# Performance work log

Hardware: AMD Instinct MI355X
Metric: run time of the kernel (lower is better)

## Reference

```python
import jax, jax.numpy as jnp
import numpy as np

N_NODES = 100000
N_EDGES = 1600000
MIN_NORM = 1e-15
BALL_EPS = 1e-5  # stay strictly inside the unit ball


def _norm(x):
    return jnp.linalg.norm(x, axis=-1, keepdims=True)


def artanh(x):
    return jnp.arctanh(jnp.clip(x, -1.0 + BALL_EPS, 1.0 - BALL_EPS))


def proj(x):
    n = jnp.maximum(_norm(x), MIN_NORM)
    maxn = 1.0 - BALL_EPS
    return jnp.where(n > maxn, x / n * maxn, x)


def expmap0(u):
    n = jnp.maximum(_norm(u), MIN_NORM)
    return jnp.tanh(n) * u / n


def logmap0(x):
    n = jnp.maximum(_norm(x), MIN_NORM)
    return artanh(n) * x / n


def mobius_add(x, y):
    x2 = jnp.sum(x * x, -1, keepdims=True)
    y2 = jnp.sum(y * y, -1, keepdims=True)
    xy = jnp.sum(x * y, -1, keepdims=True)
    num = (1.0 + 2.0 * xy + y2) * x + (1.0 - x2) * y
    den = 1.0 + 2.0 * xy + x2 * y2
    return num / jnp.maximum(den, MIN_NORM)


def mobius_matvec(W, x):
    mx = x @ W.T
    xn = jnp.maximum(_norm(x), MIN_NORM)
    mxn = jnp.maximum(_norm(mx), MIN_NORM)
    return jnp.tanh(mxn / xn * artanh(xn)) * mx / mxn


def hyp_layer(x, W, b, edge_index, use_act, use_agg):
    h = proj(mobius_matvec(W, x))
    h = proj(mobius_add(h, expmap0(b)[None, :]))
    if use_agg:
        src, dst = edge_index[0], edge_index[1]
        t = logmap0(h)                       # tangent space at origin
        msg = t[src]                         # [E, d] gather
        agg = jax.ops.segment_sum(msg, dst, num_segments=N_NODES)
        deg = jax.ops.segment_sum(jnp.ones((edge_index.shape[1],), t.dtype),
                                  dst, num_segments=N_NODES)
        agg = agg / jnp.maximum(deg, 1.0)[:, None]   # mean aggregation
        h = proj(expmap0(agg))
    if use_act:
        h = proj(expmap0(jax.nn.relu(logmap0(h))))
    return h


def lorentz_to_poincare(x):
    return x[:, 1:] / (x[:, :1] + 1.0)


def setup_inputs() -> dict:
    key = jax.random.key(0)
    ks = jax.random.split(key, 16)
    d_in, h1, d_out = 64, 64, 32
    # valid hyperboloid points: x0 = sqrt(1 + |xs|^2)
    xs = 0.1 * jax.random.normal(ks[0], (N_NODES, d_in - 1), jnp.float32)
    x0 = jnp.sqrt(1.0 + jnp.sum(xs * xs, -1, keepdims=True))
    x = jnp.concatenate([x0, xs], axis=-1)
    edge_index = jax.random.randint(ks[1], (2, N_EDGES), 0, N_NODES, jnp.int64)

    def lin(k, o, i):
        return jax.random.normal(k, (o, i), jnp.float32) * (1.0 / np.sqrt(i))

    return {
        "x": x,
        "W1": lin(ks[2], h1, d_in - 1), "b1": jnp.zeros((h1,), jnp.float32),
        "W2": lin(ks[3], h1, h1),       "b2": jnp.zeros((h1,), jnp.float32),
        "W3": lin(ks[4], h1, h1),       "b3": jnp.zeros((h1,), jnp.float32),
        "W4": lin(ks[5], h1, h1),       "b4": jnp.zeros((h1,), jnp.float32),
        "W5": lin(ks[6], h1, h1),       "b5": jnp.zeros((h1,), jnp.float32),
        "W6": lin(ks[7], d_out, h1),    "b6": jnp.zeros((d_out,), jnp.float32),
        "edge_index": edge_index,
    }


def reference(x, W1, b1, W2, b2, W3, b3, W4, b4, W5, b5, W6, b6, edge_index):
    h = proj(lorentz_to_poincare(x))
    h = hyp_layer(h, W1, b1, edge_index, use_act=True,  use_agg=False)  # hconv1
    h = hyp_layer(h, W2, b2, edge_index, use_act=True,  use_agg=False)  # hconv_2
    h = hyp_layer(h, W3, b3, edge_index, use_act=True,  use_agg=False)  # hconv_3
    h = hyp_layer(h, W4, b4, edge_index, use_act=True,  use_agg=True)   # hconv2
    h = hyp_layer(h, W5, b5, edge_index, use_act=True,  use_agg=True)   # hconv3
    h = hyp_layer(h, W6, b6, edge_index, use_act=False, use_agg=False)  # hconv4
    return h
```

## Files before the change

kernel.cpp:

```cpp
#include <hip/hip_runtime.h>
#include <hip/hip_fp16.h>

#define NN 100000
#define NE 1600000
#define TILES 6250
#define MIN_NORM 1e-15f
#define BALL_EPS 1e-5f
#define MAXN (1.0f - BALL_EPS)

#define BSH 9
#define NB 196
#define CH 8192
#define MAXB 16384

typedef __attribute__((ext_vector_type(8))) short bf16x8;
typedef __attribute__((ext_vector_type(4))) float f32x4;


__device__ __forceinline__ float rcpf(float x) { return __builtin_amdgcn_rcpf(x); }

__device__ __forceinline__ float ftanh(float x) {
    float e = __expf(-2.0f * x);
    return (1.0f - e) * rcpf(1.0f + e);
}

__device__ __forceinline__ float fatanh_c(float x) {
    x = fminf(fmaxf(x, -MAXN), MAXN);
    return 0.5f * __logf((1.0f + x) * rcpf(1.0f - x));
}


__device__ __forceinline__ float wred(float x) {
    int t;
    t = __builtin_amdgcn_update_dpp(0, __float_as_int(x), 0x111, 0xf, 0xf, false);
    x += __int_as_float(t);
    t = __builtin_amdgcn_update_dpp(0, __float_as_int(x), 0x112, 0xf, 0xf, false);
    x += __int_as_float(t);
    t = __builtin_amdgcn_update_dpp(0, __float_as_int(x), 0x114, 0xf, 0xf, false);
    x += __int_as_float(t);
    t = __builtin_amdgcn_update_dpp(0, __float_as_int(x), 0x118, 0xf, 0xf, false);
    x += __int_as_float(t);
    t = __builtin_amdgcn_update_dpp(0, __float_as_int(x), 0x142, 0xa, 0xf, false);
    x += __int_as_float(t);
    t = __builtin_amdgcn_update_dpp(0, __float_as_int(x), 0x143, 0xc, 0xf, false);
    x += __int_as_float(t);
    return __int_as_float(__builtin_amdgcn_readlane(__float_as_int(x), 63));
}

__device__ __forceinline__ float red16(float x) {
    int t;
    t = __builtin_amdgcn_update_dpp(0, __float_as_int(x), 0xB1, 0xf, 0xf, false);
    x += __int_as_float(t);
    t = __builtin_amdgcn_update_dpp(0, __float_as_int(x), 0x4E, 0xf, 0xf, false);
    x += __int_as_float(t);
    t = __builtin_amdgcn_ds_swizzle(__float_as_int(x), 0x101F);
    x += __int_as_float(t);
    t = __builtin_amdgcn_ds_swizzle(__float_as_int(x), 0x201F);
    x += __int_as_float(t);
    return x;
}


__global__ __launch_bounds__(256) void prep_w(const float* __restrict__ W1,
                                              const float* __restrict__ W2,
                                              const float* __restrict__ W3,
                                              const float* __restrict__ W4,
                                              const float* __restrict__ W5,
                                              const float* __restrict__ W6,
                                              short* __restrict__ wsplit) {
    int m = blockIdx.y;
    const float* Ws[6] = {W1, W2, W3, W4, W5, W6};
    const int dins[6] = {63, 64, 64, 64, 64, 64};
    const int douts[6] = {64, 64, 64, 64, 64, 32};
    const float* W = Ws[m];
    int din = dins[m], dout = douts[m];
    int idx = blockIdx.x * 256 + threadIdx.x;
    int j = idx >> 6, k = idx & 63;
    float x = (j < dout && k < din) ? W[j * din + k] : 0.0f;
    unsigned u = __float_as_uint(x);
    float r = x - __uint_as_float(u & 0xFFFF0000u);
    wsplit[m * 8192 + idx] = (short)(u >> 16);
    wsplit[m * 8192 + 4096 + idx] = (short)(__float_as_uint(r) >> 16);
}


__global__ __launch_bounds__(256) void l2p_kernel(const float* __restrict__ x,
                                                  float* __restrict__ out) {
    int lane = threadIdx.x & 63;
    int gw = blockIdx.x * (blockDim.x >> 6) + (threadIdx.x >> 6);
    int nw = gridDim.x * (blockDim.x >> 6);
    for (int node = gw; node < NN; node += nw) {
        float x0 = x[node * 64];
        float p = 0.0f;
        if (lane < 63) p = x[node * 64 + 1 + lane] * rcpf(x0 + 1.0f);
        float n = fmaxf(sqrtf(wred(p * p)), MIN_NORM);
        if (n > MAXN) p = p * (MAXN * rcpf(n));
        out[node * 64 + lane] = p;
    }
}

template <int MODE, int NT>
__global__ __launch_bounds__(256, 3) void layer_mfma(const float* __restrict__ in,
                                                     const short* __restrict__ wsp,
                                                     const float* __restrict__ b,
                                                     void* __restrict__ outv) {
    const int dout = NT * 16;
    float* outf = (float*)outv;
    __half* outh = (__half*)outv;
    int tid = threadIdx.x;
    int lane = tid & 63;
    int q = lane >> 4;
    int m15 = lane & 15;
    int wv = (blockIdx.x * 256 + tid) >> 6;
    int nwave = (gridDim.x * 256) >> 6;

    bf16x8 wb1[NT][2], wb2[NT][2];
#pragma unroll
    for (int t = 0; t < NT; ++t)
#pragma unroll
        for (int s = 0; s < 2; ++s) {
            int off = (16 * t + m15) * 64 + 32 * s + 8 * q;
            wb1[t][s] = *(const bf16x8*)(wsp + off);
            wb2[t][s] = *(const bf16x8*)(wsp + 4096 + off);
        }

    float bv[NT], bp = 0.0f;
#pragma unroll
    for (int t = 0; t < NT; ++t) {
        bv[t] = b[16 * t + m15];
        bp = fmaf(bv[t], bv[t], bp);
    }
    float bsum = red16(bp);
    bool bnz = (bsum > 0.0f);
    float ybt[NT] = {}; float y2 = 0.0f;
    if (bnz) {
        float bn = fmaxf(sqrtf(bsum), MIN_NORM);
        float fy = ftanh(bn) * rcpf(bn);
#pragma unroll
        for (int t = 0; t < NT; ++t) ybt[t] = fy * bv[t];
        y2 = fy * fy * bsum;
    }

    for (int tt = wv; tt < TILES; tt += nwave) {
        int base = tt * 16;
        const float* vrow = in + (size_t)(base + m15) * 64;

        bf16x8 a1[2], a2[2];
        float svp = 0.0f;
#pragma unroll
        for (int s = 0; s < 2; ++s) {
            float4 u0 = *(const float4*)(vrow + 32 * s + 8 * q);
            float4 u1 = *(const float4*)(vrow + 32 * s + 8 * q + 4);
            float f[8] = {u0.x, u0.y, u0.z, u0.w, u1.x, u1.y, u1.z, u1.w};
#pragma unroll
            for (int j = 0; j < 8; ++j) {
                svp = fmaf(f[j], f[j], svp);
                unsigned u = __float_as_uint(f[j]);
                a1[s][j] = (short)(u >> 16);
                float r = f[j] - __uint_as_float(u & 0xFFFF0000u);
                a2[s][j] = (short)(__float_as_uint(r) >> 16);
            }
        }
        float sv = svp;
        sv += __shfl_xor(sv, 16);
        sv += __shfl_xor(sv, 32);

        f32x4 acc[NT];
#pragma unroll
        for (int t = 0; t < NT; ++t) acc[t] = (f32x4){0.f, 0.f, 0.f, 0.f};
#pragma unroll
        for (int t = 0; t < NT; ++t)
#pragma unroll
            for (int s = 0; s < 2; ++s) {
                acc[t] = __builtin_amdgcn_mfma_f32_16x16x32_bf16(a1[s], wb1[t][s], acc[t], 0, 0, 0);
                acc[t] = __builtin_amdgcn_mfma_f32_16x16x32_bf16(a1[s], wb2[t][s], acc[t], 0, 0, 0);
                acc[t] = __builtin_amdgcn_mfma_f32_16x16x32_bf16(a2[s], wb1[t][s], acc[t], 0, 0, 0);
            }

        float sm[4], svr[4];
#pragma unroll
        for (int r = 0; r < 4; ++r) {
            float p = 0.0f;
#pragma unroll
            for (int t = 0; t < NT; ++t) p = fmaf(acc[t][r], acc[t][r], p);
            sm[r] = red16(p);
            svr[r] = __shfl(sv, 4 * q + r);
        }

        float o[NT][4];
#pragma unroll
        for (int r = 0; r < 4; ++r) {
            float xn = fmaxf(sqrtf(svr[r]), MIN_NORM);
            float mxn = fmaxf(sqrtf(sm[r]), MIN_NORM);
            float s1 = fminf(ftanh(mxn * rcpf(xn) * fatanh_c(xn)), MAXN);
            float fr = s1 * rcpf(mxn);
            float hv[NT];
#pragma unroll
            for (int t = 0; t < NT; ++t) hv[t] = acc[t][r] * fr;
            float hn = s1;

            if (bnz) {
                float hp = 0.0f;
#pragma unroll
                for (int t = 0; t < NT; ++t) hp = fmaf(hv[t], ybt[t], hp);
                float hy = red16(hp);
                float h2 = s1 * s1;
                float den = fmaxf(1.0f + 2.0f * hy + h2 * y2, MIN_NORM);
                float rd = rcpf(den);
                float cA = (1.0f + 2.0f * hy + y2) * rd;
                float cB = (1.0f - h2) * rd;
                float hq = 0.0f;
#pragma unroll
                for (int t = 0; t < NT; ++t) {
                    hv[t] = cA * hv[t] + cB * ybt[t];
                    hq = fmaf(hv[t], hv[t], hq);
                }
                hn = fmaxf(sqrtf(red16(hq)), MIN_NORM);
            }

            if (MODE == 2) {
                float f2 = fminf(hn, MAXN) * rcpf(hn);
#pragma unroll
                for (int t = 0; t < NT; ++t) o[t][r] = hv[t] * f2;
            } else {
                float nn = fminf(hn, MAXN);
                float tf = fatanh_c(nn) * rcpf(hn);
                if (MODE == 1) {
#pragma unroll
                    for (int t = 0; t < NT; ++t) o[t][r] = tf * hv[t];
                } else {
                    float tv[NT], tp = 0.0f;
#pragma unroll
                    for (int t = 0; t < NT; ++t) {
                        tv[t] = fmaxf(tf * hv[t], 0.0f);
                        tp = fmaf(tv[t], tv[t], tp);
                    }
                    float tn = fmaxf(sqrtf(red16(tp)), MIN_NORM);
                    float g = fminf(ftanh(tn), MAXN) * rcpf(tn);
#pragma unroll
                    for (int t = 0; t < NT; ++t) o[t][r] = tv[t] * g;
                }
            }
        }

        if (MODE == 1) {
#pragma unroll
            for (int t = 0; t < NT; ++t)
#pragma unroll
                for (int r = 0; r < 4; ++r)
                    outh[(size_t)(base + 4 * q + r) * 64 + 16 * t + m15] = __float2half(o[t][r]);
        } else {
#pragma unroll
            for (int t = 0; t < NT; ++t)
#pragma unroll
                for (int r = 0; r < 4; ++r)
                    outf[(size_t)(base + 4 * q + r) * dout + 16 * t + m15] = o[t][r];
        }
    }
}


__global__ __launch_bounds__(256) void p0_hist(const int* __restrict__ ei,
                                               int* __restrict__ ghist) {
    __shared__ int h[NB];
    for (int i = threadIdx.x; i < NB; i += 256) h[i] = 0;
    __syncthreads();
    int stride = gridDim.x * 256;
    for (int e = blockIdx.x * 256 + threadIdx.x; e < NE; e += stride)
        atomicAdd(&h[ei[NE + e] >> BSH], 1);
    __syncthreads();
    for (int i = threadIdx.x; i < NB; i += 256)
        if (h[i]) atomicAdd(&ghist[i], h[i]);
}

__global__ __launch_bounds__(256) void p_scan(const int* __restrict__ ghist,
                                              int* __restrict__ boff,
                                              int* __restrict__ bcur,
                                              int* __restrict__ rowptr) {
    __shared__ int lds[256];
    int t = threadIdx.x;
    int v = (t < NB) ? ghist[t] : 0;
    lds[t] = v;
    __syncthreads();
    for (int off = 1; off < 256; off <<= 1) {
        int u = (t >= off) ? lds[t - off] : 0;
        __syncthreads();
        lds[t] += u;
        __syncthreads();
    }
    if (t < NB) { boff[t] = lds[t] - v; bcur[t] = lds[t] - v; }
    if (t == NB - 1) boff[NB] = lds[t];
    if (t == 0) rowptr[NN] = NE;
}

__global__ __launch_bounds__(256) void p1_part(const int* __restrict__ ei,
                                               int* __restrict__ bcur,
                                               unsigned* __restrict__ packed) {
    __shared__ int hist[NB], excl[NB], cur[NB], gbase[NB];
    __shared__ int scan[256];
    __shared__ unsigned buf[CH];
    __shared__ unsigned char bseg[CH];
    int t = threadIdx.x;
    int e0 = blockIdx.x * CH;
    int n = min(CH, NE - e0);

    for (int i = t; i < NB; i += 256) hist[i] = 0;
    __syncthreads();
    for (int i = t; i < n; i += 256)
        atomicAdd(&hist[ei[NE + e0 + i] >> BSH], 1);
    __syncthreads();
    int v = (t < NB) ? hist[t] : 0;
    scan[t] = v;
    __syncthreads();
    for (int off = 1; off < 256; off <<= 1) {
        int u = (t >= off) ? scan[t - off] : 0;
        __syncthreads();
        scan[t] += u;
        __syncthreads();
    }
    if (t < NB) {
        excl[t] = scan[t] - v;
        cur[t] = scan[t] - v;
        gbase[t] = v ? atomicAdd(&bcur[t], v) : 0;
    }
    __syncthreads();
    for (int i = t; i < n; i += 256) {
        int src = ei[e0 + i], dst = ei[NE + e0 + i];
        int b = dst >> BSH;
        int p = atomicAdd(&cur[b], 1);
        buf[p] = ((unsigned)(dst & 511) << 17) | (unsigned)src;
        bseg[p] = (unsigned char)b;
    }
    __syncthreads();
    for (int i = t; i < n; i += 256) {
        int b = bseg[i];
        packed[gbase[b] + (i - excl[b])] = buf[i];
    }
}

__global__ __launch_bounds__(512) void p2_csr(const unsigned* __restrict__ packed,
                                              const int* __restrict__ boff,
                                              int* __restrict__ rowptr,
                                              int* __restrict__ csr) {
    __shared__ int lh[512], lex[512], lcur[512], scan[512];
    __shared__ int image[MAXB];
    int t = threadIdx.x;
    int b = blockIdx.x;
    int n0 = b << BSH;
    int nn = min(512, NN - n0);
    int ebeg = boff[b], eend = boff[b + 1];
    int cnt = eend - ebeg;

    lh[t] = 0;
    __syncthreads();
    for (int i = t; i < cnt; i += 512)
        atomicAdd(&lh[packed[ebeg + i] >> 17], 1);
    __syncthreads();
    int v = lh[t];
    scan[t] = v;
    __syncthreads();
    for (int off = 1; off < 512; off <<= 1) {
        int u = (t >= off) ? scan[t - off] : 0;
        __syncthreads();
        scan[t] += u;
        __syncthreads();
    }
    lex[t] = scan[t] - v;
    lcur[t] = scan[t] - v;
    if (t < nn) rowptr[n0 + t] = ebeg + lex[t];
    __syncthreads();
    for (int i = t; i < cnt; i += 512) {
        unsigned p = packed[ebeg + i];
        int pos = atomicAdd(&lcur[p >> 17], 1);
        image[pos] = (int)(p & 0x1FFFFu);
    }
    __syncthreads();
    for (int i = t; i < cnt; i += 512)
        csr[ebeg + i] = image[i];
}


__global__ __launch_bounds__(256) void gather_post_kernel(const __half* __restrict__ t16,
                                                          const int* __restrict__ rowptr,
                                                          const int* __restrict__ csr,
                                                          float* __restrict__ out) {
    int lane = threadIdx.x & 63;
    int g = lane >> 4;
    int l16 = lane & 15;
    int dq = l16 << 2;
    int gw = blockIdx.x * (blockDim.x >> 6) + (threadIdx.x >> 6);
    int nw = gridDim.x * (blockDim.x >> 6);
    for (int node = gw; node < NN; node += nw) {
        int beg = __builtin_amdgcn_readfirstlane(rowptr[node]);
        int end = __builtin_amdgcn_readfirstlane(rowptr[node + 1]);
        float ax = 0.f, ay = 0.f, az = 0.f, aw = 0.f;
        float bx = 0.f, by = 0.f, bz = 0.f, bw = 0.f;
        int i = beg;
        for (; i + 8 <= end; i += 8) {
            int sA = csr[i + g];
            int sB = csr[i + 4 + g];
            uint2 uA = *(const uint2*)(t16 + ((sA << 6) + dq));
            uint2 uB = *(const uint2*)(t16 + ((sB << 6) + dq));
            float2 fA0 = __half22float2(*(const half2*)&uA.x);
            float2 fA1 = __half22float2(*(const half2*)&uA.y);
            float2 fB0 = __half22float2(*(const half2*)&uB.x);
            float2 fB1 = __half22float2(*(const half2*)&uB.y);
            ax += fA0.x; ay += fA0.y; az += fA1.x; aw += fA1.y;
            bx += fB0.x; by += fB0.y; bz += fB1.x; bw += fB1.y;
        }
        for (; i < end; i += 4) {
            int idx = i + g;
            if (idx < end) {
                int s = csr[idx];
                uint2 u = *(const uint2*)(t16 + ((s << 6) + dq));
                float2 f0 = __half22float2(*(const half2*)&u.x);
                float2 f1 = __half22float2(*(const half2*)&u.y);
                ax += f0.x; ay += f0.y; az += f1.x; aw += f1.y;
            }
        }
        ax += bx; ay += by; az += bz; aw += bw;
        ax += __shfl_xor(ax, 16); ax += __shfl_xor(ax, 32);
        ay += __shfl_xor(ay, 16); ay += __shfl_xor(ay, 32);
        az += __shfl_xor(az, 16); az += __shfl_xor(az, 32);
        aw += __shfl_xor(aw, 16); aw += __shfl_xor(aw, 32);
        float rdeg = rcpf(fmaxf((float)(end - beg), 1.0f));
        ax *= rdeg; ay *= rdeg; az *= rdeg; aw *= rdeg;

        float p = fmaf(ax, ax, fmaf(ay, ay, fmaf(az, az, aw * aw)));
        p = red16(p);
        float n = fmaxf(sqrtf(p), MIN_NORM);
        float s = fminf(ftanh(n), MAXN);
        float c = fatanh_c(s) * rcpf(s) * (s * rcpf(n));
        float tx = fmaxf(c * ax, 0.f), ty = fmaxf(c * ay, 0.f);
        float tz = fmaxf(c * az, 0.f), tw = fmaxf(c * aw, 0.f);
        float tp = fmaf(tx, tx, fmaf(ty, ty, fmaf(tz, tz, tw * tw)));
        tp = red16(tp);
        float tn = fmaxf(sqrtf(tp), MIN_NORM);
        float g2 = fminf(ftanh(tn), MAXN) * rcpf(tn);
        if (g == 0) {
            float4 o = {tx * g2, ty * g2, tz * g2, tw * g2};
            *(float4*)(out + (size_t)node * 64 + dq) = o;
        }
    }
}


extern "C" void kernel_launch(void* const* d_in, const int* in_sizes, int n_in,
                              void* d_out, int out_size, void* d_ws, size_t ws_size,
                              hipStream_t stream) {
    const float* x  = (const float*)d_in[0];
    const float* W1 = (const float*)d_in[1];  const float* b1 = (const float*)d_in[2];
    const float* W2 = (const float*)d_in[3];  const float* b2 = (const float*)d_in[4];
    const float* W3 = (const float*)d_in[5];  const float* b3 = (const float*)d_in[6];
    const float* W4 = (const float*)d_in[7];  const float* b4 = (const float*)d_in[8];
    const float* W5 = (const float*)d_in[9];  const float* b5 = (const float*)d_in[10];
    const float* W6 = (const float*)d_in[11]; const float* b6 = (const float*)d_in[12];
    const int*   ei = (const int*)d_in[13];
    float* out = (float*)d_out;

    float*    A      = (float*)d_ws;
    float*    B      = A + (size_t)NN * 64;
    __half*   T16    = (__half*)(B + (size_t)NN * 64);
    int*      csr    = (int*)(T16 + (size_t)NN * 64);
    int*      rowptr = csr + NE;
    unsigned* packed = (unsigned*)(rowptr + NN + 1);
    int*      ghist  = (int*)(packed + NE);
    int*      boff   = ghist + NB;
    int*      bcur   = boff + NB + 1;
    short*    wsplit = (short*)(bcur + NB);

    dim3 blk(256);
    const int lg = 768;
    const int ng = 1024;
    const int gg = 2048;
    const int p1g = (NE + CH - 1) / CH;

    prep_w<<<dim3(16, 6), blk, 0, stream>>>(W1, W2, W3, W4, W5, W6, wsplit);
    hipMemsetAsync(ghist, 0, NB * sizeof(int), stream);
    p0_hist<<<512, blk, 0, stream>>>(ei, ghist);
    p_scan<<<1, blk, 0, stream>>>(ghist, boff, bcur, rowptr);
    p1_part<<<p1g, blk, 0, stream>>>(ei, bcur, packed);
    p2_csr<<<NB, 512, 0, stream>>>(packed, boff, rowptr, csr);

    l2p_kernel<<<ng, blk, 0, stream>>>(x, A);

    layer_mfma<0, 4><<<lg, blk, 0, stream>>>(A, wsplit + 0 * 8192, b1, B);
    layer_mfma<0, 4><<<lg, blk, 0, stream>>>(B, wsplit + 1 * 8192, b2, A);
    layer_mfma<0, 4><<<lg, blk, 0, stream>>>(A, wsplit + 2 * 8192, b3, B);

    layer_mfma<1, 4><<<lg, blk, 0, stream>>>(B, wsplit + 3 * 8192, b4, T16);
    gather_post_kernel<<<gg, blk, 0, stream>>>(T16, rowptr, csr, B);

    layer_mfma<1, 4><<<lg, blk, 0, stream>>>(B, wsplit + 4 * 8192, b5, T16);
    gather_post_kernel<<<gg, blk, 0, stream>>>(T16, rowptr, csr, B);

    layer_mfma<2, 2><<<lg, blk, 0, stream>>>(B, wsplit + 5 * 8192, b6, out);
}
```

Before: 364.4 us.

## Store activations as pre-split bf16 hi/lo with cached norms and artanh

Inter-layer activations are now written as pre-split bf16 hi/lo planes plus a per-node (norm, artanh(norm)) pair, so each layer loads MFMA operands directly instead of reloading fp32 and splitting them. The norm and artanh are computed once by the producer. The code also uses the algebraic identity artanh(tanh(z)) = z, clamped at ZMAX, to skip the tanh/artanh round trips when the bias is zero and in the gather epilogue. The split does not change activation bytes and adds a small norm side buffer. The shortcut depends on the clamp constant matching the reference clipping, and the packed buffer now aliases T16.

```diff
diff --git a/kernel.cpp b/kernel.cpp
--- a/kernel.cpp
+++ b/kernel.cpp
@@ -7,6 +7,7 @@
 #define MIN_NORM 1e-15f
 #define BALL_EPS 1e-5f
 #define MAXN (1.0f - BALL_EPS)
+#define ZMAX 6.1030338f
 
 #define BSH 9
 #define NB 196
@@ -14,6 +15,7 @@
 #define MAXB 16384
 
 typedef __attribute__((ext_vector_type(8))) short bf16x8;
+typedef __attribute__((ext_vector_type(4))) short short4v;
 typedef __attribute__((ext_vector_type(4))) float f32x4;
 
 
@@ -27,6 +29,13 @@
 __device__ __forceinline__ float fatanh_c(float x) {
     x = fminf(fmaxf(x, -MAXN), MAXN);
     return 0.5f * __logf((1.0f + x) * rcpf(1.0f - x));
+}
+
+__device__ __forceinline__ void bsplit(float v, short& hi, short& lo) {
+    unsigned u = __float_as_uint(v);
+    hi = (short)(u >> 16);
+    float r = v - __uint_as_float(u & 0xFFFF0000u);
+    lo = (short)(__float_as_uint(r) >> 16);
 }
 
 
@@ -77,15 +86,17 @@
     int idx = blockIdx.x * 256 + threadIdx.x;
     int j = idx >> 6, k = idx & 63;
     float x = (j < dout && k < din) ? W[j * din + k] : 0.0f;
-    unsigned u = __float_as_uint(x);
-    float r = x - __uint_as_float(u & 0xFFFF0000u);
-    wsplit[m * 8192 + idx] = (short)(u >> 16);
-    wsplit[m * 8192 + 4096 + idx] = (short)(__float_as_uint(r) >> 16);
+    short hi, lo;
+    bsplit(x, hi, lo);
+    wsplit[m * 8192 + idx] = hi;
+    wsplit[m * 8192 + 4096 + idx] = lo;
 }
 
 
 __global__ __launch_bounds__(256) void l2p_kernel(const float* __restrict__ x,
-                                                  float* __restrict__ out) {
+                                                  short* __restrict__ outHi,
+                                                  short* __restrict__ outLo,
+                                                  float2* __restrict__ outNrm) {
     int lane = threadIdx.x & 63;
     int gw = blockIdx.x * (blockDim.x >> 6) + (threadIdx.x >> 6);
     int nw = gridDim.x * (blockDim.x >> 6);
@@ -95,18 +106,29 @@
         if (lane < 63) p = x[node * 64 + 1 + lane] * rcpf(x0 + 1.0f);
         float n = fmaxf(sqrtf(wred(p * p)), MIN_NORM);
         if (n > MAXN) p = p * (MAXN * rcpf(n));
-        out[node * 64 + lane] = p;
+        short hi, lo;
+        bsplit(p, hi, lo);
+        outHi[node * 64 + lane] = hi;
+        outLo[node * 64 + lane] = lo;
+        if (lane == 0) {
+            float xn = fminf(n, MAXN);
+            outNrm[node] = make_float2(xn, fatanh_c(xn));
+        }
     }
 }
 
 template <int MODE, int NT>
-__global__ __launch_bounds__(256, 3) void layer_mfma(const float* __restrict__ in,
+__global__ __launch_bounds__(256, 3) void layer_mfma(const short* __restrict__ inHi,
+                                                     const short* __restrict__ inLo,
+                                                     const float2* __restrict__ inNrm,
                                                      const short* __restrict__ wsp,
                                                      const float* __restrict__ b,
-                                                     void* __restrict__ outv) {
+                                                     short* __restrict__ outHi,
+                                                     short* __restrict__ outLo,
+                                                     float2* __restrict__ outNrm,
+                                                     __half* __restrict__ outT,
+                                                     float* __restrict__ outF) {
     const int dout = NT * 16;
-    float* outf = (float*)outv;
-    __half* outh = (__half*)outv;
     int tid = threadIdx.x;
     int lane = tid & 63;
     int q = lane >> 4;
@@ -143,27 +165,15 @@
 
     for (int tt = wv; tt < TILES; tt += nwave) {
         int base = tt * 16;
-        const float* vrow = in + (size_t)(base + m15) * 64;
+        int rowoff = (base + m15) * 64;
 
         bf16x8 a1[2], a2[2];
-        float svp = 0.0f;
 #pragma unroll
         for (int s = 0; s < 2; ++s) {
-            float4 u0 = *(const float4*)(vrow + 32 * s + 8 * q);
-            float4 u1 = *(const float4*)(vrow + 32 * s + 8 * q + 4);
-            float f[8] = {u0.x, u0.y, u0.z, u0.w, u1.x, u1.y, u1.z, u1.w};
-#pragma unroll
-            for (int j = 0; j < 8; ++j) {
-                svp = fmaf(f[j], f[j], svp);
-                unsigned u = __float_as_uint(f[j]);
-                a1[s][j] = (short)(u >> 16);
-                float r = f[j] - __uint_as_float(u & 0xFFFF0000u);
-                a2[s][j] = (short)(__float_as_uint(r) >> 16);
-            }
-        }
-        float sv = svp;
-        sv += __shfl_xor(sv, 16);
-        sv += __shfl_xor(sv, 32);
+            a1[s] = *(const bf16x8*)(inHi + rowoff + 32 * s + 8 * q);
+            a2[s] = *(const bf16x8*)(inLo + rowoff + 32 * s + 8 * q);
+        }
+        float2 nrm = inNrm[base + m15];
 
         f32x4 acc[NT];
 #pragma unroll
@@ -177,34 +187,73 @@
                 acc[t] = __builtin_amdgcn_mfma_f32_16x16x32_bf16(a2[s], wb1[t][s], acc[t], 0, 0, 0);
             }
 
-        float sm[4], svr[4];
+        float sm[4];
 #pragma unroll
         for (int r = 0; r < 4; ++r) {
             float p = 0.0f;
 #pragma unroll
             for (int t = 0; t < NT; ++t) p = fmaf(acc[t][r], acc[t][r], p);
             sm[r] = red16(p);
-            svr[r] = __shfl(sv, 4 * q + r);
-        }
-
-        float o[NT][4];
+        }
+
 #pragma unroll
         for (int r = 0; r < 4; ++r) {
-            float xn = fmaxf(sqrtf(svr[r]), MIN_NORM);
+            int nd = base + 4 * q + r;
+            float xn = __shfl(nrm.x, 4 * q + r);
+            float axn = __shfl(nrm.y, 4 * q + r);
             float mxn = fmaxf(sqrtf(sm[r]), MIN_NORM);
-            float s1 = fminf(ftanh(mxn * rcpf(xn) * fatanh_c(xn)), MAXN);
-            float fr = s1 * rcpf(mxn);
-            float hv[NT];
-#pragma unroll
-            for (int t = 0; t < NT; ++t) hv[t] = acc[t][r] * fr;
-            float hn = s1;
-
-            if (bnz) {
+            float z = mxn * rcpf(xn) * axn;
+            float az = fminf(z, ZMAX);
+
+            if (!bnz) {
+                if (MODE == 2) {
+                    float e = __expf(-2.0f * z);
+                    float s1c = fminf((1.0f - e) * rcpf(1.0f + e), MAXN);
+                    float fr = s1c * rcpf(mxn);
+#pragma unroll
+                    for (int t = 0; t < NT; ++t)
+                        outF[(size_t)nd * dout + 16 * t + m15] = acc[t][r] * fr;
+                } else {
+                    float tfac = az * rcpf(mxn);
+                    if (MODE == 1) {
+#pragma unroll
+                        for (int t = 0; t < NT; ++t)
+                            outT[(size_t)nd * 64 + 16 * t + m15] = __float2half(tfac * acc[t][r]);
+                    } else {
+                        float tv[NT], tp = 0.0f;
+#pragma unroll
+                        for (int t = 0; t < NT; ++t) {
+                            tv[t] = fmaxf(tfac * acc[t][r], 0.0f);
+                            tp = fmaf(tv[t], tv[t], tp);
+                        }
+                        float tn = fmaxf(sqrtf(red16(tp)), MIN_NORM);
+                        float e2 = __expf(-2.0f * tn);
+                        float s2c = fminf((1.0f - e2) * rcpf(1.0f + e2), MAXN);
+                        float g = s2c * rcpf(tn);
+#pragma unroll
+                        for (int t = 0; t < NT; ++t) {
+                            short hi, lo;
+                            bsplit(tv[t] * g, hi, lo);
+                            int idx = nd * 64 + 16 * t + m15;
+                            outHi[idx] = hi;
+                            outLo[idx] = lo;
+                        }
+                        if (m15 == 0)
+                            outNrm[nd] = make_float2(fmaxf(s2c, MIN_NORM), fminf(tn, ZMAX));
+                    }
+                }
+            } else {
+                float e = __expf(-2.0f * z);
+                float s1c = fminf((1.0f - e) * rcpf(1.0f + e), MAXN);
+                float fr = s1c * rcpf(mxn);
+                float hv[NT];
+#pragma unroll
+                for (int t = 0; t < NT; ++t) hv[t] = acc[t][r] * fr;
                 float hp = 0.0f;
 #pragma unroll
                 for (int t = 0; t < NT; ++t) hp = fmaf(hv[t], ybt[t], hp);
                 float hy = red16(hp);
-                float h2 = s1 * s1;
+                float h2 = s1c * s1c;
                 float den = fmaxf(1.0f + 2.0f * hy + h2 * y2, MIN_NORM);
                 float rd = rcpf(den);
                 float cA = (1.0f + 2.0f * hy + y2) * rd;
@@ -215,46 +264,41 @@
                     hv[t] = cA * hv[t] + cB * ybt[t];
                     hq = fmaf(hv[t], hv[t], hq);
                 }
-                hn = fmaxf(sqrtf(red16(hq)), MIN_NORM);
-            }
-
-            if (MODE == 2) {
-                float f2 = fminf(hn, MAXN) * rcpf(hn);
-#pragma unroll
-                for (int t = 0; t < NT; ++t) o[t][r] = hv[t] * f2;
-            } else {
-                float nn = fminf(hn, MAXN);
-                float tf = fatanh_c(nn) * rcpf(hn);
-                if (MODE == 1) {
-#pragma unroll
-                    for (int t = 0; t < NT; ++t) o[t][r] = tf * hv[t];
+                float hn = fmaxf(sqrtf(red16(hq)), MIN_NORM);
+                if (MODE == 2) {
+                    float f2 = fminf(hn, MAXN) * rcpf(hn);
+#pragma unroll
+                    for (int t = 0; t < NT; ++t)
+                        outF[(size_t)nd * dout + 16 * t + m15] = hv[t] * f2;
                 } else {
-                    float tv[NT], tp = 0.0f;
-#pragma unroll
-                    for (int t = 0; t < NT; ++t) {
-                        tv[t] = fmaxf(tf * hv[t], 0.0f);
-                        tp = fmaf(tv[t], tv[t], tp);
+                    float tf = fatanh_c(fminf(hn, MAXN)) * rcpf(hn);
+                    if (MODE == 1) {
+#pragma unroll
+                        for (int t = 0; t < NT; ++t)
+                            outT[(size_t)nd * 64 + 16 * t + m15] = __float2half(tf * hv[t]);
+                    } else {
+                        float tv[NT], tp = 0.0f;
+#pragma unroll
+                        for (int t = 0; t < NT; ++t) {
+                            tv[t] = fmaxf(tf * hv[t], 0.0f);
+                            tp = fmaf(tv[t], tv[t], tp);
+                        }
+                        float tn = fmaxf(sqrtf(red16(tp)), MIN_NORM);
+                        float s2c = fminf(ftanh(tn), MAXN);
+                        float g = s2c * rcpf(tn);
+#pragma unroll
+                        for (int t = 0; t < NT; ++t) {
+                            short hi, lo;
+                            bsplit(tv[t] * g, hi, lo);
+                            int idx = nd * 64 + 16 * t + m15;
+                            outHi[idx] = hi;
+                            outLo[idx] = lo;
+                        }
+                        if (m15 == 0)
+                            outNrm[nd] = make_float2(fmaxf(s2c, MIN_NORM), fminf(tn, ZMAX));
                     }
-                    float tn = fmaxf(sqrtf(red16(tp)), MIN_NORM);
-                    float g = fminf(ftanh(tn), MAXN) * rcpf(tn);
-#pragma unroll
-                    for (int t = 0; t < NT; ++t) o[t][r] = tv[t] * g;
                 }
             }
-        }
-
-        if (MODE == 1) {
-#pragma unroll
-            for (int t = 0; t < NT; ++t)
-#pragma unroll
-                for (int r = 0; r < 4; ++r)
-                    outh[(size_t)(base + 4 * q + r) * 64 + 16 * t + m15] = __float2half(o[t][r]);
-        } else {
-#pragma unroll
-            for (int t = 0; t < NT; ++t)
-#pragma unroll
-                for (int r = 0; r < 4; ++r)
-                    outf[(size_t)(base + 4 * q + r) * dout + 16 * t + m15] = o[t][r];
         }
     }
 }
@@ -383,7 +427,9 @@
 __global__ __launch_bounds__(256) void gather_post_kernel(const __half* __restrict__ t16,
                                                           const int* __restrict__ rowptr,
                                                           const int* __restrict__ csr,
-                                                          float* __restrict__ out) {
+                                                          short* __restrict__ outHi,
+                                                          short* __restrict__ outLo,
+                                                          float2* __restrict__ outNrm) {
     int lane = threadIdx.x & 63;
     int g = lane >> 4;
     int l16 = lane & 15;
@@ -429,17 +475,24 @@
         float p = fmaf(ax, ax, fmaf(ay, ay, fmaf(az, az, aw * aw)));
         p = red16(p);
         float n = fmaxf(sqrtf(p), MIN_NORM);
-        float s = fminf(ftanh(n), MAXN);
-        float c = fatanh_c(s) * rcpf(s) * (s * rcpf(n));
+        float c = (n > ZMAX) ? (ZMAX * rcpf(n)) : 1.0f;
         float tx = fmaxf(c * ax, 0.f), ty = fmaxf(c * ay, 0.f);
         float tz = fmaxf(c * az, 0.f), tw = fmaxf(c * aw, 0.f);
         float tp = fmaf(tx, tx, fmaf(ty, ty, fmaf(tz, tz, tw * tw)));
         tp = red16(tp);
         float tn = fmaxf(sqrtf(tp), MIN_NORM);
-        float g2 = fminf(ftanh(tn), MAXN) * rcpf(tn);
+        float e2 = __expf(-2.0f * tn);
+        float s2c = fminf((1.0f - e2) * rcpf(1.0f + e2), MAXN);
+        float g2 = s2c * rcpf(tn);
         if (g == 0) {
-            float4 o = {tx * g2, ty * g2, tz * g2, tw * g2};
-            *(float4*)(out + (size_t)node * 64 + dq) = o;
+            float o[4] = {tx * g2, ty * g2, tz * g2, tw * g2};
+            short4v hi, lo;
+#pragma unroll
+            for (int j = 0; j < 4; ++j) { short h, l; bsplit(o[j], h, l); hi[j] = h; lo[j] = l; }
+            *(short4v*)(outHi + node * 64 + dq) = hi;
+            *(short4v*)(outLo + node * 64 + dq) = lo;
+            if (l16 == 0)
+                outNrm[node] = make_float2(fmaxf(s2c, MIN_NORM), fminf(tn, ZMAX));
         }
     }
 }
@@ -458,16 +511,21 @@
     const int*   ei = (const int*)d_in[13];
     float* out = (float*)d_out;
 
-    float*    A      = (float*)d_ws;
-    float*    B      = A + (size_t)NN * 64;
-    __half*   T16    = (__half*)(B + (size_t)NN * 64);
-    int*      csr    = (int*)(T16 + (size_t)NN * 64);
-    int*      rowptr = csr + NE;
-    unsigned* packed = (unsigned*)(rowptr + NN + 1);
-    int*      ghist  = (int*)(packed + NE);
-    int*      boff   = ghist + NB;
-    int*      bcur   = boff + NB + 1;
-    short*    wsplit = (short*)(bcur + NB);
+    char* w = (char*)d_ws;
+    short*   AHi  = (short*)w;            w += (size_t)NN * 64 * 2;
+    short*   ALo  = (short*)w;            w += (size_t)NN * 64 * 2;
+    short*   BHi  = (short*)w;            w += (size_t)NN * 64 * 2;
+    short*   BLo  = (short*)w;            w += (size_t)NN * 64 * 2;
+    float2*  Anrm = (float2*)w;           w += (size_t)NN * 8;
+    float2*  Bnrm = (float2*)w;           w += (size_t)NN * 8;
+    __half*  T16  = (__half*)w;           w += (size_t)NN * 64 * 2;
+    unsigned* packed = (unsigned*)T16;
+    int*     csr    = (int*)w;            w += (size_t)NE * 4;
+    int*     rowptr = (int*)w;            w += (size_t)(NN + 1) * 4;
+    int*     ghist  = (int*)w;            w += NB * 4;
+    int*     boff   = (int*)w;            w += (NB + 1) * 4;
+    int*     bcur   = (int*)w;            w += NB * 4;
+    short*   wsplit = (short*)w;
 
     dim3 blk(256);
     const int lg = 768;
@@ -482,17 +540,23 @@
     p1_part<<<p1g, blk, 0, stream>>>(ei, bcur, packed);
     p2_csr<<<NB, 512, 0, stream>>>(packed, boff, rowptr, csr);
 
-    l2p_kernel<<<ng, blk, 0, stream>>>(x, A);
-
-    layer_mfma<0, 4><<<lg, blk, 0, stream>>>(A, wsplit + 0 * 8192, b1, B);
-    layer_mfma<0, 4><<<lg, blk, 0, stream>>>(B, wsplit + 1 * 8192, b2, A);
-    layer_mfma<0, 4><<<lg, blk, 0, stream>>>(A, wsplit + 2 * 8192, b3, B);
-
-    layer_mfma<1, 4><<<lg, blk, 0, stream>>>(B, wsplit + 3 * 8192, b4, T16);
-    gather_post_kernel<<<gg, blk, 0, stream>>>(T16, rowptr, csr, B);
-
-    layer_mfma<1, 4><<<lg, blk, 0, stream>>>(B, wsplit + 4 * 8192, b5, T16);
-    gather_post_kernel<<<gg, blk, 0, stream>>>(T16, rowptr, csr, B);
-
-    layer_mfma<2, 2><<<lg, blk, 0, stream>>>(B, wsplit + 5 * 8192, b6, out);
-}
+    l2p_kernel<<<ng, blk, 0, stream>>>(x, AHi, ALo, Anrm);
+
+    layer_mfma<0, 4><<<lg, blk, 0, stream>>>(AHi, ALo, Anrm, wsplit + 0 * 8192, b1,
+                                             BHi, BLo, Bnrm, nullptr, nullptr);
+    layer_mfma<0, 4><<<lg, blk, 0, stream>>>(BHi, BLo, Bnrm, wsplit + 1 * 8192, b2,
+                                             AHi, ALo, Anrm, nullptr, nullptr);
+    layer_mfma<0, 4><<<lg, blk, 0, stream>>>(AHi, ALo, Anrm, wsplit + 2 * 8192, b3,
+                                             BHi, BLo, Bnrm, nullptr, nullptr);
+
+    layer_mfma<1, 4><<<lg, blk, 0, stream>>>(BHi, BLo, Bnrm, wsplit + 3 * 8192, b4,
+                                             nullptr, nullptr, nullptr, T16, nullptr);
+    gather_post_kernel<<<gg, blk, 0, stream>>>(T16, rowptr, csr, AHi, ALo, Anrm);
+
+    layer_mfma<1, 4><<<lg, blk, 0, stream>>>(AHi, ALo, Anrm, wsplit + 4 * 8192, b5,
+                                             nullptr, nullptr, nullptr, T16, nullptr);
+    gather_post_kernel<<<gg, blk, 0, stream>>>(T16, rowptr, csr, BHi, BLo, Bnrm);
+
+    layer_mfma<2, 2><<<lg, blk, 0, stream>>>(BHi, BLo, Bnrm, wsplit + 5 * 8192, b6,
+                                             nullptr, nullptr, nullptr, nullptr, out);
+}
```

New measurement: 359.0 us. Within noise of the previous version (-1.5%).
